# Kernel optimization log

Measured on AMD Instinct MI355X. Metric: run time of the kernel, lower is better.

The kernel has to match this reference:

```python
import math
import jax, jax.numpy as jnp
import numpy as np

C, H, R, PD = 256, 6, 32, 16
HEAD_SCALE = 1.0 / math.sqrt(R)


def setup_inputs() -> dict:
    key = jax.random.key(0)
    ks = jax.random.split(key, 8)
    B, Lp1 = 8, 4097
    feats = jax.random.normal(ks[0], (B, Lp1, C), dtype=jnp.float32)
    # params (stored [in, out] for x @ W)
    Wq = jax.random.normal(ks[1], (C, H * R), dtype=jnp.float32) / math.sqrt(C)
    Wk = jax.random.normal(ks[2], (C, H * R), dtype=jnp.float32) / math.sqrt(C)
    Wpi = jax.random.normal(ks[3], (C, PD), dtype=jnp.float32) / math.sqrt(C)
    bpi = jnp.zeros((PD,), jnp.float32)
    Wpj = jax.random.normal(ks[4], (C, PD), dtype=jnp.float32) / math.sqrt(C)
    bpj = jnp.zeros((PD,), jnp.float32)
    Wd = jax.random.normal(ks[5], (C, 1), dtype=jnp.float32) / math.sqrt(C)
    bd = jnp.zeros((1,), jnp.float32)
    alpha_pair = jnp.float32(0.5)
    logit_scale = jnp.float32(1.0)
    return {"feats": feats, "Wq": Wq, "Wk": Wk, "Wpi": Wpi, "bpi": bpi,
            "Wpj": Wpj, "bpj": bpj, "Wd": Wd, "bd": bd,
            "alpha_pair": alpha_pair, "logit_scale": logit_scale}


def _fold_vertices(feats):
    x = feats[:, 1:]                      # drop first token
    B, L, Cc = x.shape
    return x.reshape(B, L // 2, 2, Cc).mean(axis=2)  # [B, N, C]


def reference(feats, Wq, Wk, Wpi, bpi, Wpj, bpj, Wd, bd, alpha_pair, logit_scale):
    x = _fold_vertices(feats)             # [B, N, C]
    B, N, _ = x.shape
    Q = (x @ Wq).reshape(B, N, H, R)
    K = (x @ Wk).reshape(B, N, H, R)
    # sum over heads fused into one contraction (math-equal to per-head scores summed)
    S = jnp.einsum('bnhr,bmhr->bnm', Q, K) * HEAD_SCALE   # [B, N, N]
    a_i = jax.nn.relu(x @ Wpi + bpi)      # [B, N, PD]
    b_j = jax.nn.relu(x @ Wpj + bpj)
    S = S + jnp.maximum(alpha_pair, 0.0) * jnp.einsum('bnd,bmd->bnm', a_i, b_j)
    d = (x @ Wd + bd)[..., 0]             # [B, N]
    idx = jnp.arange(N)
    S = S.at[:, idx, idx].add(d)
    return S * jnp.maximum(logit_scale, 0.01)
```

## Files before the change

kernel.cpp:

```cpp
#include <hip/hip_runtime.h>
#include <hip/hip_bf16.h>
#include <stdint.h>

typedef __attribute__((ext_vector_type(8))) short short8;
typedef __attribute__((ext_vector_type(4))) short short4v;
typedef __attribute__((ext_vector_type(4))) float f32x4;
typedef __attribute__((ext_vector_type(4))) unsigned uint4v;

#define NB 8
#define NN 2048
#define CC 256
#define LP1 4097
#define HR 192
#define PDim 16
#define KP 224
#define NPAD 448
#define HEAD_SCALE 0.17677669529663689f

#define GLOAD16(g, l) __builtin_amdgcn_global_load_lds( \
    (const __attribute__((address_space(1))) unsigned int*)(g), \
    (__attribute__((address_space(3))) unsigned int*)(l), 16, 0, 0)

static __device__ __forceinline__ unsigned short bf16bits(float f) {
    __hip_bfloat16 h = __float2bfloat16(f);
    return *(unsigned short*)&h;
}

__global__ __launch_bounds__(256) void k0_prep(
    const float* __restrict__ Wq, const float* __restrict__ Wk,
    const float* __restrict__ Wpi, const float* __restrict__ Wpj,
    const float* __restrict__ Wd,
    __hip_bfloat16* __restrict__ WT,
    unsigned* __restrict__ Ppad, unsigned* __restrict__ Rpad)
{
    const int WTN = NPAD*CC;
    const int PV  = NB*NN*2;
    int i = blockIdx.x*blockDim.x + threadIdx.x;
    if (i < WTN) {
        int c = i >> 8, k = i & 255;
        float v;
        if (c < HR)                 v = Wq[k*HR + c] * HEAD_SCALE;
        else if (c < 2*HR)          v = Wk[k*HR + (c-HR)];
        else if (c < 2*HR+PDim)     v = Wpi[k*PDim + (c-2*HR)];
        else if (c < 2*HR+2*PDim)   v = Wpj[k*PDim + (c-2*HR-PDim)];
        else if (c == 416)          v = Wd[k];
        else                        v = 0.f;
        WT[i] = __float2bfloat16(v);
    } else {
        int j = i - WTN;
        unsigned* arr = (j < PV) ? Ppad : Rpad;
        int q = (j < PV) ? j : j - PV;
        int row = q >> 1, of = 104 + (q & 1)*4;
        *(uint4v*)(arr + (size_t)row*(KP/2) + of) = (uint4v){0,0,0,0};
    }
}

__global__ __launch_bounds__(256, 3) void ka_proj(
    const float* __restrict__ feats, const __hip_bfloat16* __restrict__ WT,
    const float* __restrict__ bpi, const float* __restrict__ bpj,
    const float* __restrict__ bd, const float* __restrict__ alpha_pair,
    __hip_bfloat16* __restrict__ P, __hip_bfloat16* __restrict__ R,
    float* __restrict__ dvec)
{
    __shared__ __hip_bfloat16 lds[32*256];

    int t = threadIdx.x;
    int lane = t & 63;
    int w = t >> 6;
    int l15 = lane & 15, lg = lane >> 4;
    int row0 = blockIdx.x * 32;
    int b = row0 >> 11;
    int n0loc = row0 & (NN-1);

    {
        int r = t >> 3, cg = t & 7;
        size_t fb = ((size_t)b*LP1 + 1 + 2*(size_t)(n0loc + r))*CC + cg*32;
#pragma unroll
        for (int s = 0; s < 4; ++s) {
            float4 a0 = *(const float4*)(feats + fb + s*8);
            float4 a1 = *(const float4*)(feats + fb + s*8 + 4);
            float4 c0 = *(const float4*)(feats + fb + CC + s*8);
            float4 c1 = *(const float4*)(feats + fb + CC + s*8 + 4);
            unsigned short h[8];
            h[0] = bf16bits(0.5f*(a0.x + c0.x));
            h[1] = bf16bits(0.5f*(a0.y + c0.y));
            h[2] = bf16bits(0.5f*(a0.z + c0.z));
            h[3] = bf16bits(0.5f*(a0.w + c0.w));
            h[4] = bf16bits(0.5f*(a1.x + c1.x));
            h[5] = bf16bits(0.5f*(a1.y + c1.y));
            h[6] = bf16bits(0.5f*(a1.z + c1.z));
            h[7] = bf16bits(0.5f*(a1.w + c1.w));
            int slot = (cg*4 + s) ^ (r & 7);
            *(short8*)((char*)lds + r*512 + slot*16) = *(const short8*)h;
        }
    }
    __syncthreads();

    const __hip_bfloat16* pB[7];
#pragma unroll
    for (int ni = 0; ni < 7; ++ni)
        pB[ni] = WT + (size_t)(w*112 + ni*16 + l15)*CC + lg*8;

    f32x4 acc[7][2];
#pragma unroll
    for (int ni = 0; ni < 7; ++ni)
#pragma unroll
        for (int mi = 0; mi < 2; ++mi)
            acc[ni][mi] = (f32x4){0.f, 0.f, 0.f, 0.f};

    int arow[2];
#pragma unroll
    for (int mi = 0; mi < 2; ++mi) arow[mi] = (mi*16 + l15)*512;
    int rx = l15 & 7;

#pragma unroll
    for (int kk = 0; kk < 8; ++kk) {
        short8 a[2], bb[7];
        int slotb = ((kk*4 + lg) ^ rx) << 4;
#pragma unroll
        for (int mi = 0; mi < 2; ++mi)
            a[mi] = *(const short8*)((const char*)lds + arow[mi] + slotb);
#pragma unroll
        for (int ni = 0; ni < 7; ++ni) bb[ni] = *(const short8*)(pB[ni] + kk*32);
#pragma unroll
        for (int ni = 0; ni < 7; ++ni)
#pragma unroll
            for (int mi = 0; mi < 2; ++mi)
                acc[ni][mi] = __builtin_amdgcn_mfma_f32_16x16x32_bf16(
                    bb[ni], a[mi], acc[ni][mi], 0, 0, 0);
    }

    float alpha_eff = fmaxf(alpha_pair[0], 0.f);
    float bd0 = bd[0];
#pragma unroll
    for (int ni = 0; ni < 7; ++ni) {
        int cb = w*112 + ni*16 + lg*4;
#pragma unroll
        for (int mi = 0; mi < 2; ++mi) {
            int n = n0loc + mi*16 + l15;
            size_t rb = ((size_t)b*NN + n)*KP;
            f32x4 v = acc[ni][mi];
            if (cb < HR) {
                short4v h;
#pragma unroll
                for (int j = 0; j < 4; ++j) h[j] = (short)bf16bits(v[j]);
                *(short4v*)(P + rb + cb) = h;
            } else if (cb < 2*HR) {
                short4v h;
#pragma unroll
                for (int j = 0; j < 4; ++j) h[j] = (short)bf16bits(v[j]);
                *(short4v*)(R + rb + (cb - HR)) = h;
            } else if (cb < 2*HR + PDim) {
                int pc = cb - 2*HR;
                short4v h;
#pragma unroll
                for (int j = 0; j < 4; ++j)
                    h[j] = (short)bf16bits(fmaxf(v[j] + bpi[pc+j], 0.f) * alpha_eff);
                *(short4v*)(P + rb + HR + pc) = h;
            } else if (cb < 2*HR + 2*PDim) {
                int pc = cb - 2*HR - PDim;
                short4v h;
#pragma unroll
                for (int j = 0; j < 4; ++j)
                    h[j] = (short)bf16bits(fmaxf(v[j] + bpj[pc+j], 0.f));
                *(short4v*)(R + rb + HR + pc) = h;
            } else if (cb == 416) {
                dvec[(size_t)b*NN + n] = v[0] + bd0;
            }
        }
    }
}

__global__ __launch_bounds__(512, 2) void kb_pair(
    const __hip_bfloat16* __restrict__ P, const __hip_bfloat16* __restrict__ R,
    const float* __restrict__ dvec, const float* __restrict__ logit_scale,
    float* __restrict__ out)
{
    __shared__ __hip_bfloat16 ldsA[2][256*32];
    __shared__ __hip_bfloat16 ldsB[2][256*32];

    int t = threadIdx.x;
    int lane = t & 63;
    int w = t >> 6;
    int wr = w >> 1, wc = w & 1;
    int l15 = lane & 15, lg = lane >> 4;

    int hw = blockIdx.x;
    int b = hw & 7;
    int within = hw >> 3;
    int m0 = (within & 7) << 8;
    int n0 = (within >> 3) << 8;

    const char* srcA[2];
    const char* srcB[2];
#pragma unroll
    for (int i = 0; i < 2; ++i) {
        int row   = i*128 + (t >> 2);
        int scolb = ((t & 3) << 4) ^ ((row & 3) << 4);
        srcA[i] = (const char*)(P + ((size_t)b*NN + n0 + row)*KP) + scolb;
        srcB[i] = (const char*)(R + ((size_t)b*NN + m0 + row)*KP) + scolb;
    }
    char* A0 = (char*)&ldsA[0][0];
    char* B0 = (char*)&ldsB[0][0];
    int ldst = w * 1024;

    int abyte = (wr*64  + l15)*64 + ((lg ^ (l15 & 3)) << 4);
    int bbyte = (wc*128 + l15)*64 + ((lg ^ (l15 & 3)) << 4);

    f32x4 acc[8][4];
#pragma unroll
    for (int ni = 0; ni < 8; ++ni)
#pragma unroll
        for (int mi = 0; mi < 4; ++mi)
            acc[ni][mi] = (f32x4){0.f, 0.f, 0.f, 0.f};

#pragma unroll
    for (int i = 0; i < 2; ++i) {
        GLOAD16(srcA[i], A0 + i*8192 + ldst);
        GLOAD16(srcB[i], B0 + i*8192 + ldst);
    }
#pragma unroll
    for (int i = 0; i < 2; ++i) {
        GLOAD16(srcA[i] + 64, A0 + 16384 + i*8192 + ldst);
        GLOAD16(srcB[i] + 64, B0 + 16384 + i*8192 + ldst);
    }

#pragma unroll
    for (int s = 0; s < 7; ++s) {
        if (s < 6) asm volatile("s_waitcnt vmcnt(4)" ::: "memory");
        else       asm volatile("s_waitcnt vmcnt(0)" ::: "memory");
        __builtin_amdgcn_s_barrier();
        __builtin_amdgcn_sched_barrier(0);

        const int buf = s & 1;
        short8 a[4], bb[8];
#pragma unroll
        for (int mi = 0; mi < 4; ++mi)
            a[mi] = *(const short8*)(A0 + buf*16384 + abyte + mi*1024);
#pragma unroll
        for (int ni = 0; ni < 8; ++ni)
            bb[ni] = *(const short8*)(B0 + buf*16384 + bbyte + ni*1024);
#pragma unroll
        for (int ni = 0; ni < 8; ++ni)
#pragma unroll
            for (int mi = 0; mi < 4; ++mi)
                acc[ni][mi] = __builtin_amdgcn_mfma_f32_16x16x32_bf16(
                    bb[ni], a[mi], acc[ni][mi], 0, 0, 0);

        __builtin_amdgcn_sched_barrier(0);
        __builtin_amdgcn_s_barrier();
        if (s + 2 < 7) {
            size_t kof = (size_t)(s + 2) * 64;
#pragma unroll
            for (int i = 0; i < 2; ++i) {
                GLOAD16(srcA[i] + kof, A0 + buf*16384 + i*8192 + ldst);
                GLOAD16(srcB[i] + kof, B0 + buf*16384 + i*8192 + ldst);
            }
        }
    }

    float ls = fmaxf(logit_scale[0], 0.01f);
    bool diag_tile = (n0 == m0);
#pragma unroll
    for (int ni = 0; ni < 8; ++ni) {
#pragma unroll
        for (int mi = 0; mi < 4; ++mi) {
            int orow  = n0 + wr*64  + mi*16 + l15;
            int cbase = m0 + wc*128 + ni*16 + lg*4;
            f32x4 v = acc[ni][mi];
            if (diag_tile) {
                int dj = orow - cbase;
                if (dj >= 0 && dj < 4) v[dj] += dvec[(size_t)b*NN + orow];
            }
            f32x4 o;
#pragma unroll
            for (int j = 0; j < 4; ++j) o[j] = v[j] * ls;
            *(f32x4*)(out + ((size_t)b*NN + orow)*NN + cbase) = o;
        }
    }
}

extern "C" void kernel_launch(void* const* d_in, const int* in_sizes, int n_in,
                              void* d_out, int out_size, void* d_ws, size_t ws_size,
                              hipStream_t stream)
{
    const float* feats = (const float*)d_in[0];
    const float* Wq    = (const float*)d_in[1];
    const float* Wk    = (const float*)d_in[2];
    const float* Wpi   = (const float*)d_in[3];
    const float* bpi   = (const float*)d_in[4];
    const float* Wpj   = (const float*)d_in[5];
    const float* bpj   = (const float*)d_in[6];
    const float* Wd    = (const float*)d_in[7];
    const float* bd    = (const float*)d_in[8];
    const float* alpha = (const float*)d_in[9];
    const float* lsc   = (const float*)d_in[10];

    char* ws = (char*)d_ws;
    __hip_bfloat16* WT = (__hip_bfloat16*)(ws);
    __hip_bfloat16* P  = (__hip_bfloat16*)(ws + 229376);
    __hip_bfloat16* R  = (__hip_bfloat16*)(ws + 7569408);
    float*          dv = (float*)(ws + 14909440);

    k0_prep<<<704, 256, 0, stream>>>(Wq, Wk, Wpi, Wpj, Wd,
                                     WT, (unsigned*)P, (unsigned*)R);
    ka_proj<<<512, 256, 0, stream>>>(feats, WT, bpi, bpj, bd, alpha, P, R, dv);
    kb_pair<<<512, 512, 0, stream>>>(P, R, dv, lsc, (float*)d_out);
}
```

Baseline: 69.85 us.

## Stage projection weights through LDS and change LDS swizzle in score GEMM

In the projection kernel, weight tiles are now loaded cooperatively into LDS with register prefetch of the next k-slice, replacing per-wave direct global loads of B fragments. Block indexing is reordered so the batch index varies fastest. The score kernel's LDS swizzle is changed from row&3 to (row>>2)&3 to reduce bank conflicts on fragment reads. The added per-iteration barriers and extra LDS traffic may offset the gains in the small projection kernel.

```diff
diff --git a/kernel.cpp b/kernel.cpp
--- a/kernel.cpp
+++ b/kernel.cpp
@@ -62,15 +62,30 @@
     __hip_bfloat16* __restrict__ P, __hip_bfloat16* __restrict__ R,
     float* __restrict__ dvec)
 {
-    __shared__ __hip_bfloat16 lds[32*256];
+    __shared__ __hip_bfloat16 ldsA[32*256];
+    __shared__ __hip_bfloat16 ldsB[448*32];
 
     int t = threadIdx.x;
     int lane = t & 63;
     int w = t >> 6;
     int l15 = lane & 15, lg = lane >> 4;
-    int row0 = blockIdx.x * 32;
-    int b = row0 >> 11;
-    int n0loc = row0 & (NN-1);
+    int hw = blockIdx.x;
+    int b = hw & 7;
+    int n0loc = (hw >> 3) * 32;
+
+    int scol = (((t & 3) ^ ((t >> 4) & 3)) << 4);
+    const char* srcB[7];
+    int wofB[7];
+#pragma unroll
+    for (int i = 0; i < 7; ++i) {
+        int row = i*64 + (t >> 2);
+        srcB[i] = (const char*)WT + (size_t)row*512 + scol;
+        wofB[i] = row*64 + ((t & 3) << 4);
+    }
+
+    uint4v st[7];
+#pragma unroll
+    for (int i = 0; i < 7; ++i) st[i] = *(const uint4v*)(srcB[i]);
 
     {
         int r = t >> 3, cg = t & 7;
@@ -91,15 +106,14 @@
             h[6] = bf16bits(0.5f*(a1.z + c1.z));
             h[7] = bf16bits(0.5f*(a1.w + c1.w));
             int slot = (cg*4 + s) ^ (r & 7);
-            *(short8*)((char*)lds + r*512 + slot*16) = *(const short8*)h;
-        }
-    }
+            *(short8*)((char*)ldsA + r*512 + slot*16) = *(const short8*)h;
+        }
+    }
+
+#pragma unroll
+    for (int i = 0; i < 7; ++i)
+        *(uint4v*)((char*)ldsB + wofB[i]) = st[i];
     __syncthreads();
-
-    const __hip_bfloat16* pB[7];
-#pragma unroll
-    for (int ni = 0; ni < 7; ++ni)
-        pB[ni] = WT + (size_t)(w*112 + ni*16 + l15)*CC + lg*8;
 
     f32x4 acc[7][2];
 #pragma unroll
@@ -112,22 +126,37 @@
 #pragma unroll
     for (int mi = 0; mi < 2; ++mi) arow[mi] = (mi*16 + l15)*512;
     int rx = l15 & 7;
+    int bbase = (w*112 + l15)*64 + ((lg ^ ((l15 >> 2) & 3)) << 4);
 
 #pragma unroll
     for (int kk = 0; kk < 8; ++kk) {
+        if (kk < 7) {
+#pragma unroll
+            for (int i = 0; i < 7; ++i)
+                st[i] = *(const uint4v*)(srcB[i] + (size_t)(kk + 1)*64);
+        }
         short8 a[2], bb[7];
         int slotb = ((kk*4 + lg) ^ rx) << 4;
 #pragma unroll
         for (int mi = 0; mi < 2; ++mi)
-            a[mi] = *(const short8*)((const char*)lds + arow[mi] + slotb);
-#pragma unroll
-        for (int ni = 0; ni < 7; ++ni) bb[ni] = *(const short8*)(pB[ni] + kk*32);
+            a[mi] = *(const short8*)((const char*)ldsA + arow[mi] + slotb);
+#pragma unroll
+        for (int ni = 0; ni < 7; ++ni)
+            bb[ni] = *(const short8*)((const char*)ldsB + bbase + ni*1024);
 #pragma unroll
         for (int ni = 0; ni < 7; ++ni)
 #pragma unroll
             for (int mi = 0; mi < 2; ++mi)
                 acc[ni][mi] = __builtin_amdgcn_mfma_f32_16x16x32_bf16(
                     bb[ni], a[mi], acc[ni][mi], 0, 0, 0);
+
+        __syncthreads();
+        if (kk < 7) {
+#pragma unroll
+            for (int i = 0; i < 7; ++i)
+                *(uint4v*)((char*)ldsB + wofB[i]) = st[i];
+            __syncthreads();
+        }
     }
 
     float alpha_eff = fmaxf(alpha_pair[0], 0.f);
@@ -193,19 +222,21 @@
 
     const char* srcA[2];
     const char* srcB[2];
-#pragma unroll
-    for (int i = 0; i < 2; ++i) {
-        int row   = i*128 + (t >> 2);
-        int scolb = ((t & 3) << 4) ^ ((row & 3) << 4);
-        srcA[i] = (const char*)(P + ((size_t)b*NN + n0 + row)*KP) + scolb;
-        srcB[i] = (const char*)(R + ((size_t)b*NN + m0 + row)*KP) + scolb;
+    {
+        int scolb = (((t & 3) ^ ((t >> 4) & 3)) << 4);
+#pragma unroll
+        for (int i = 0; i < 2; ++i) {
+            int row = i*128 + (t >> 2);
+            srcA[i] = (const char*)(P + ((size_t)b*NN + n0 + row)*KP) + scolb;
+            srcB[i] = (const char*)(R + ((size_t)b*NN + m0 + row)*KP) + scolb;
+        }
     }
     char* A0 = (char*)&ldsA[0][0];
     char* B0 = (char*)&ldsB[0][0];
     int ldst = w * 1024;
 
-    int abyte = (wr*64  + l15)*64 + ((lg ^ (l15 & 3)) << 4);
-    int bbyte = (wc*128 + l15)*64 + ((lg ^ (l15 & 3)) << 4);
+    int abyte = (wr*64  + l15)*64 + ((lg ^ ((l15 >> 2) & 3)) << 4);
+    int bbyte = (wc*128 + l15)*64 + ((lg ^ ((l15 >> 2) & 3)) << 4);
 
     f32x4 acc[8][4];
 #pragma unroll
```

After: 64.84 us. 1.08x faster.
